# Kernel optimization log

Measured on AMD Instinct MI355X. Metric: run time of the kernel, lower is better.

Reference implementation:

```python
import jax, jax.numpy as jnp
import numpy as np

N_NODES = 100000
N_EDGES = 1600000
IN_DIM, HID_DIM, OUT_DIM = 128, 64, 32
NEG_SLOPE = 0.2  # PyG GATConv default negative_slope


def gat_conv(x, src, dst, num_nodes, W, a_src, a_dst, bias):
    # x: [N, in], W: [in, out], a_src/a_dst: [out], bias: [out]
    h = x @ W                                        # [N, out]
    alpha_s = h @ a_src                              # [N] per-node source score
    alpha_d = h @ a_dst                              # [N] per-node target score
    e = jax.nn.leaky_relu(alpha_s[src] + alpha_d[dst], NEG_SLOPE)  # [E]
    # segment softmax over incoming edges of each dst node
    m = jax.ops.segment_max(e, dst, num_segments=num_nodes)        # [N]
    ex = jnp.exp(e - m[dst])                                        # [E]
    z = jax.ops.segment_sum(ex, dst, num_segments=num_nodes)        # [N]
    coef = ex / z[dst]                                              # [E]
    out = jax.ops.segment_sum(coef[:, None] * h[src], dst, num_segments=num_nodes)
    return out + bias


def setup_inputs() -> dict:
    key = jax.random.key(0)
    ks = jax.random.split(key, 10)
    x = jax.random.normal(ks[0], (N_NODES, IN_DIM), dtype=jnp.float32)
    edge_index = jax.random.randint(ks[1], (2, N_EDGES), 0, N_NODES, dtype=jnp.int64)
    s = 0.1
    W1 = jax.random.normal(ks[2], (IN_DIM, HID_DIM), dtype=jnp.float32) * s
    a_src1 = jax.random.normal(ks[3], (HID_DIM,), dtype=jnp.float32) * s
    a_dst1 = jax.random.normal(ks[4], (HID_DIM,), dtype=jnp.float32) * s
    b1 = jnp.zeros((HID_DIM,), dtype=jnp.float32)
    W2 = jax.random.normal(ks[5], (HID_DIM, OUT_DIM), dtype=jnp.float32) * s
    a_src2 = jax.random.normal(ks[6], (OUT_DIM,), dtype=jnp.float32) * s
    a_dst2 = jax.random.normal(ks[7], (OUT_DIM,), dtype=jnp.float32) * s
    b2 = jnp.zeros((OUT_DIM,), dtype=jnp.float32)
    return {"x": x, "edge_index": edge_index, "W1": W1, "a_src1": a_src1,
            "a_dst1": a_dst1, "b1": b1, "W2": W2, "a_src2": a_src2,
            "a_dst2": a_dst2, "b2": b2}


def reference(x, edge_index, W1, a_src1, a_dst1, b1, W2, a_src2, a_dst2, b2):
    n = x.shape[0]
    loops = jnp.arange(n, dtype=edge_index.dtype)
    src = jnp.concatenate([edge_index[0], loops])  # add_self_loops=True default
    dst = jnp.concatenate([edge_index[1], loops])
    h = jax.nn.relu(gat_conv(x, src, dst, n, W1, a_src1, a_dst1, b1))
    out = gat_conv(h, src, dst, n, W2, a_src2, a_dst2, b2)
    return jax.nn.log_softmax(out, axis=1)
```

## Files before the change

### kernel.cpp

```cpp
#include <hip/hip_runtime.h>

#define N_NODES 100000
#define N_EDGES 1600000
#define ET (N_EDGES + N_NODES)
#define NEG_SLOPE 0.2f

#define BSHIFT 9
#define BW 512
#define NBUCK ((N_NODES + BW - 1) / BW)
#define BCAP 10240
#define BINCH 2048

typedef unsigned short u16;
typedef unsigned int u32;

__device__ __forceinline__ float bf2f(u16 v) {
    return __uint_as_float(((u32)v) << 16);
}
__device__ __forceinline__ u16 f2bf(float f) {
    u32 u = __float_as_uint(f);
    u32 r = (u + 0x7FFFu + ((u >> 16) & 1u)) >> 16;
    return (u16)r;
}
__device__ __forceinline__ float lrelu(float x) { return x > 0.f ? x : NEG_SLOPE * x; }
__device__ __forceinline__ float ldf(const void* p, int i, int bf) {
    return bf ? bf2f(((const u16*)p)[i]) : ((const float*)p)[i];
}
__device__ __forceinline__ int get_dst(const int* __restrict__ ei, int e, int ei64) {
    if (e < N_EDGES) return ei64 ? ei[2 * (N_EDGES + e)] : ei[N_EDGES + e];
    return e - N_EDGES;
}
__device__ __forceinline__ int get_src(const int* __restrict__ ei, int e, int ei64) {
    if (e < N_EDGES) return ei64 ? ei[2 * e] : ei[e];
    return e - N_EDGES;
}

__device__ __forceinline__ void fma8(float wt, uint4 qv, float (&acc)[8]) {
    acc[0] = fmaf(wt, __uint_as_float(qv.x << 16), acc[0]);
    acc[1] = fmaf(wt, __uint_as_float(qv.x & 0xFFFF0000u), acc[1]);
    acc[2] = fmaf(wt, __uint_as_float(qv.y << 16), acc[2]);
    acc[3] = fmaf(wt, __uint_as_float(qv.y & 0xFFFF0000u), acc[3]);
    acc[4] = fmaf(wt, __uint_as_float(qv.z << 16), acc[4]);
    acc[5] = fmaf(wt, __uint_as_float(qv.z & 0xFFFF0000u), acc[5]);
    acc[6] = fmaf(wt, __uint_as_float(qv.w << 16), acc[6]);
    acc[7] = fmaf(wt, __uint_as_float(qv.w & 0xFFFF0000u), acc[7]);
}

__global__ void detect_kernel(const u32* __restrict__ x32, const int* __restrict__ ei,
                              int* __restrict__ flags, int* __restrict__ bcnt) {
    int lane = threadIdx.x;
    for (int i = lane; i < 256; i += 64) bcnt[i] = 0;
    u32 e = (x32[lane] >> 7) & 0xFFu;
    int ok = (e >= 96u && e <= 143u) ? 1 : 0;
    int cnt = (int)__popcll(__ballot(ok));
    int nz = (ei[2 * lane + 1] != 0) + (ei[2 * (lane + 64) + 1] != 0);
    #pragma unroll
    for (int off = 32; off > 0; off >>= 1) nz += __shfl_xor(nz, off);
    if (lane == 0) { flags[0] = (cnt >= 48) ? 1 : 0; flags[1] = (nz == 0) ? 1 : 0; }
}

__global__ __launch_bounds__(256) void bin_kernel(
    const int* __restrict__ ei, const int* __restrict__ flags,
    int* __restrict__ bcnt, u32* __restrict__ bbuf)
{
    __shared__ int hist[NBUCK];
    const int t = threadIdx.x;
    const int base = blockIdx.x * BINCH;
    const int ei64 = flags[1];
    for (int i = t; i < NBUCK; i += 256) hist[i] = 0;
    __syncthreads();
    for (int i = t; i < BINCH; i += 256) {
        int e = base + i;
        if (e >= ET) break;
        int d = get_dst(ei, e, ei64);
        atomicAdd(&hist[d >> BSHIFT], 1);
    }
    __syncthreads();
    for (int i = t; i < NBUCK; i += 256) {
        int c = hist[i];
        hist[i] = (c > 0) ? atomicAdd(&bcnt[i], c) : 0;
    }
    __syncthreads();
    for (int i = t; i < BINCH; i += 256) {
        int e = base + i;
        if (e >= ET) break;
        int d = get_dst(ei, e, ei64);
        int s = get_src(ei, e, ei64);
        int b = d >> BSHIFT;
        int pos = atomicAdd(&hist[b], 1);
        if (pos < BCAP)
            bbuf[(size_t)b * BCAP + pos] = ((u32)(d & (BW - 1)) << 17) | (u32)s;
    }
}

__global__ __launch_bounds__(256) void bscan_kernel(
    const int* __restrict__ bcnt, int* __restrict__ bbase)
{
    __shared__ int sd[256];
    int t = threadIdx.x;
    int v = (t < NBUCK) ? min(bcnt[t], BCAP) : 0;
    sd[t] = v;
    __syncthreads();
    for (int off = 1; off < 256; off <<= 1) {
        int x = (t >= off) ? sd[t - off] : 0;
        __syncthreads();
        sd[t] += x;
        __syncthreads();
    }
    if (t < NBUCK) bbase[t] = sd[t] - v;
    if (t == NBUCK - 1) bbase[NBUCK] = sd[t];
}

__global__ __launch_bounds__(1024) void scatter_kernel(
    const int* __restrict__ bcnt, const int* __restrict__ bbase,
    const u32* __restrict__ bbuf, int* __restrict__ rowptr, int* __restrict__ ssrc)
{
    __shared__ int hist[BW];
    __shared__ int cur[BW];
    __shared__ int wtot[4];
    __shared__ int lds_s[BCAP];
    const int t = threadIdx.x;
    const int b = blockIdx.x;
    const int cnt = min(bcnt[b], BCAP);
    const int base = bbase[b];
    const u32* mybuf = bbuf + (size_t)b * BCAP;

    if (t < BW) hist[t] = 0;
    __syncthreads();
    for (int i = t; i < cnt; i += 1024) atomicAdd(&hist[(int)(mybuf[i] >> 17)], 1);
    __syncthreads();
    int a0 = 0, a1 = 0, s = 0, v = 0;
    const int lane = t & 63, wid = t >> 6;
    if (t < 256) {
        a0 = hist[2 * t]; a1 = hist[2 * t + 1];
        s = a0 + a1;
        v = s;
        #pragma unroll
        for (int off = 1; off < 64; off <<= 1) {
            int n = __shfl_up(v, off);
            if (lane >= off) v += n;
        }
        if (lane == 63) wtot[wid] = v;
    }
    __syncthreads();
    if (t == 0) {
        int acc = 0;
        #pragma unroll
        for (int w = 0; w < 4; ++w) { int tmp = wtot[w]; wtot[w] = acc; acc += tmp; }
    }
    __syncthreads();
    if (t < 256) {
        int excl = v + wtot[wid] - s;
        cur[2 * t] = excl;
        cur[2 * t + 1] = excl + a0;
    }
    __syncthreads();
    if (t < BW) {
        int g = b * BW + t;
        if (g < N_NODES) rowptr[g] = base + cur[t];
    }
    if (b == NBUCK - 1 && t == 0) rowptr[N_NODES] = bbase[NBUCK];
    __syncthreads();
    for (int i = t; i < cnt; i += 1024) {
        u32 code = mybuf[i];
        int pos = atomicAdd(&cur[(int)(code >> 17)], 1);
        lds_s[pos] = (int)(code & 0x1FFFFu);
    }
    __syncthreads();
    for (int i = t; i < cnt; i += 1024) ssrc[base + i] = lds_s[i];
}

__global__ __launch_bounds__(256) void gemm1_kernel(
    const float* __restrict__ x, const float* __restrict__ W,
    const void* __restrict__ a_src, const void* __restrict__ a_dst,
    const int* __restrict__ flags,
    u16* __restrict__ h, float* __restrict__ as_, float* __restrict__ ad_)
{
    __shared__ float xs[256 * 33];
    __shared__ float Wl[32 * 64];
    const int t = threadIdx.x;
    const int node0 = blockIdx.x * 256;
    const int bf = flags[0];
    const int ng = t >> 3;
    const int cg = t & 7;

    float acc[8][8];
    #pragma unroll
    for (int i = 0; i < 8; ++i)
        #pragma unroll
        for (int j = 0; j < 8; ++j) acc[i][j] = 0.f;

    for (int kc = 0; kc < 4; ++kc) {
        const int kb = kc * 32;
        const int c4 = t & 7;
        #pragma unroll
        for (int p = 0; p < 8; ++p) {
            int row = (t >> 3) + p * 32;
            int n = node0 + row;
            float4 vv = make_float4(0.f, 0.f, 0.f, 0.f);
            if (n < N_NODES) {
                if (!bf) {
                    vv = *(const float4*)(x + (size_t)n * 128 + kb + c4 * 4);
                } else {
                    const u16* xh = (const u16*)x;
                    vv.x = bf2f(xh[(size_t)n * 128 + kb + c4 * 4 + 0]);
                    vv.y = bf2f(xh[(size_t)n * 128 + kb + c4 * 4 + 1]);
                    vv.z = bf2f(xh[(size_t)n * 128 + kb + c4 * 4 + 2]);
                    vv.w = bf2f(xh[(size_t)n * 128 + kb + c4 * 4 + 3]);
                }
            }
            float* dstp = &xs[row * 33 + c4 * 4];
            dstp[0] = vv.x; dstp[1] = vv.y; dstp[2] = vv.z; dstp[3] = vv.w;
        }
        if (!bf) {
            #pragma unroll
            for (int qq = 0; qq < 2; ++qq) {
                int f4 = t * 2 + qq;
                ((float4*)Wl)[f4] = ((const float4*)(W + (size_t)kb * 64))[f4];
            }
        } else {
            const u16* Wh = (const u16*)W;
            for (int i = t; i < 2048; i += 256) Wl[i] = bf2f(Wh[(size_t)kb * 64 + i]);
        }
        __syncthreads();

        for (int kk = 0; kk < 32; ++kk) {
            float xr[8];
            #pragma unroll
            for (int i = 0; i < 8; ++i) xr[i] = xs[(ng * 8 + i) * 33 + kk];
            float4 w0 = *(const float4*)&Wl[kk * 64 + cg * 8];
            float4 w1 = *(const float4*)&Wl[kk * 64 + cg * 8 + 4];
            const float wr[8] = {w0.x, w0.y, w0.z, w0.w, w1.x, w1.y, w1.z, w1.w};
            #pragma unroll
            for (int i = 0; i < 8; ++i)
                #pragma unroll
                for (int j = 0; j < 8; ++j)
                    acc[i][j] = fmaf(xr[i], wr[j], acc[i][j]);
        }
        __syncthreads();
    }

    float av[8], dv[8];
    #pragma unroll
    for (int j = 0; j < 8; ++j) {
        av[j] = ldf(a_src, cg * 8 + j, bf);
        dv[j] = ldf(a_dst, cg * 8 + j, bf);
    }
    #pragma unroll
    for (int i = 0; i < 8; ++i) {
        int n = node0 + ng * 8 + i;
        float ps = 0.f, pd = 0.f;
        #pragma unroll
        for (int j = 0; j < 8; ++j) { ps += acc[i][j] * av[j]; pd += acc[i][j] * dv[j]; }
        #pragma unroll
        for (int off = 1; off < 8; off <<= 1) {
            ps += __shfl_xor(ps, off);
            pd += __shfl_xor(pd, off);
        }
        if (n < N_NODES) {
            uint4 hv;
            hv.x = (u32)f2bf(acc[i][0]) | ((u32)f2bf(acc[i][1]) << 16);
            hv.y = (u32)f2bf(acc[i][2]) | ((u32)f2bf(acc[i][3]) << 16);
            hv.z = (u32)f2bf(acc[i][4]) | ((u32)f2bf(acc[i][5]) << 16);
            hv.w = (u32)f2bf(acc[i][6]) | ((u32)f2bf(acc[i][7]) << 16);
            *(uint4*)&h[(size_t)n * 64 + cg * 8] = hv;
            if (cg == 0) { as_[n] = ps; ad_[n] = pd; }
        }
    }
}

template<int SH>
__global__ __launch_bounds__(256) void score_kernel(
    const int* __restrict__ rowptr, const int* __restrict__ ssrc,
    const float* __restrict__ as_, const float* __restrict__ ad_,
    uint2* __restrict__ wexs)
{
    int d = blockIdx.x * 256 + threadIdx.x;
    if (d >= N_NODES) return;
    int beg = rowptr[d], end = rowptr[d + 1];
    int deg = end - beg;
    float add = ad_[d];

    if (deg <= 64) {
        int sj[64];
        float sc[64];
        #pragma unroll
        for (int i = 0; i < 64; ++i) {
            int j = beg + ((i < deg) ? i : 0);
            sj[i] = ssrc[j];
        }
        #pragma unroll
        for (int i = 0; i < 64; ++i) sc[i] = as_[sj[i]];
        float m = -1e30f;
        #pragma unroll
        for (int i = 0; i < 64; ++i) {
            sc[i] = lrelu(sc[i] + add);
            m = (i < deg) ? fmaxf(m, sc[i]) : m;
        }
        float l = 0.f;
        #pragma unroll
        for (int i = 0; i < 64; ++i) {
            float e = (i < deg) ? __expf(sc[i] - m) : 0.f;
            sc[i] = e;
            l += e;
        }
        float inv = 1.f / l;
        #pragma unroll
        for (int i = 0; i < 64; ++i)
            if (i < deg)
                wexs[beg + i] = make_uint2(__float_as_uint(sc[i] * inv),
                                           ((u32)sj[i]) << SH);
    } else {
        float m = -1e30f;
        for (int j = beg; j < end; ++j) m = fmaxf(m, lrelu(as_[ssrc[j]] + add));
        float l = 0.f;
        for (int j = beg; j < end; ++j) l += __expf(lrelu(as_[ssrc[j]] + add) - m);
        float inv = 1.f / l;
        for (int j = beg; j < end; ++j) {
            int s = ssrc[j];
            wexs[j] = make_uint2(
                __float_as_uint(__expf(lrelu(as_[s] + add) - m) * inv),
                ((u32)s) << SH);
        }
    }
}

__global__ __launch_bounds__(256) void gather64_kernel(
    const int* __restrict__ rowptr, const uint2* __restrict__ wexs,
    const u16* __restrict__ h, float* __restrict__ agg)
{
    const int tid = threadIdx.x;
    const int hl = tid & 31;
    const int dreal = blockIdx.x * 8 + (tid >> 5);
    const int dst = min(dreal, N_NODES - 1);
    const int beg = rowptr[dst];
    const int deg = rowptr[dst + 1] - beg;
    const int e4 = hl >> 3;
    const int i8 = hl & 7;
    const char* __restrict__ hb = (const char*)h;
    const u32 boff = (u32)(i8 * 16);

    float acc[8] = {0.f, 0.f, 0.f, 0.f, 0.f, 0.f, 0.f, 0.f};

    #pragma unroll
    for (int g = 0; g < 8; ++g) {
        int eidx = g * 4 + e4;
        bool valid = eidx < deg;
        uint2 p = wexs[beg + (valid ? eidx : 0)];
        float w = valid ? __uint_as_float(p.x) : 0.f;
        uint4 qv = *(const uint4*)(hb + (size_t)(p.y + boff));
        fma8(w, qv, acc);
    }
    int mdeg = max(deg, __shfl_xor(deg, 32));
    for (int g = 8; g * 4 < mdeg; ++g) {
        int eidx = g * 4 + e4;
        bool valid = eidx < deg;
        uint2 p = wexs[beg + (valid ? eidx : 0)];
        float w = valid ? __uint_as_float(p.x) : 0.f;
        uint4 qv = *(const uint4*)(hb + (size_t)(p.y + boff));
        fma8(w, qv, acc);
    }

    #pragma unroll
    for (int c = 0; c < 8; ++c) {
        acc[c] += __shfl_xor(acc[c], 8);
        acc[c] += __shfl_xor(acc[c], 16);
    }
    if (e4 == 0 && dreal < N_NODES) {
        *(float4*)&agg[(size_t)dst * 64 + i8 * 8] =
            make_float4(acc[0], acc[1], acc[2], acc[3]);
        *(float4*)&agg[(size_t)dst * 64 + i8 * 8 + 4] =
            make_float4(acc[4], acc[5], acc[6], acc[7]);
    }
}

__global__ __launch_bounds__(256) void gather32_lsm_kernel(
    const int* __restrict__ rowptr, const uint2* __restrict__ wexs,
    const u16* __restrict__ h, const void* __restrict__ b2,
    const int* __restrict__ flags, float* __restrict__ out)
{
    const int tid = threadIdx.x;
    const int hl = tid & 31;
    const int dreal = blockIdx.x * 8 + (tid >> 5);
    const int dst = min(dreal, N_NODES - 1);
    const int beg = rowptr[dst];
    const int deg = rowptr[dst + 1] - beg;
    const int e8 = hl >> 2;
    const int i4 = hl & 3;
    const int bf = flags[0];
    const char* __restrict__ hb = (const char*)h;
    const u32 boff = (u32)(i4 * 16);

    float acc[8] = {0.f, 0.f, 0.f, 0.f, 0.f, 0.f, 0.f, 0.f};

    #pragma unroll
    for (int g = 0; g < 4; ++g) {
        int eidx = g * 8 + e8;
        bool valid = eidx < deg;
        uint2 p = wexs[beg + (valid ? eidx : 0)];
        float w = valid ? __uint_as_float(p.x) : 0.f;
        uint4 qv = *(const uint4*)(hb + (size_t)(p.y + boff));
        fma8(w, qv, acc);
    }
    int mdeg = max(deg, __shfl_xor(deg, 32));
    for (int g = 4; g * 8 < mdeg; ++g) {
        int eidx = g * 8 + e8;
        bool valid = eidx < deg;
        uint2 p = wexs[beg + (valid ? eidx : 0)];
        float w = valid ? __uint_as_float(p.x) : 0.f;
        uint4 qv = *(const uint4*)(hb + (size_t)(p.y + boff));
        fma8(w, qv, acc);
    }

    #pragma unroll
    for (int c = 0; c < 8; ++c) {
        acc[c] += __shfl_xor(acc[c], 4);
        acc[c] += __shfl_xor(acc[c], 8);
        acc[c] += __shfl_xor(acc[c], 16);
    }

    float v[8];
    #pragma unroll
    for (int c = 0; c < 8; ++c) v[c] = acc[c] + ldf(b2, i4 * 8 + c, bf);
    float mx = v[0];
    #pragma unroll
    for (int c = 1; c < 8; ++c) mx = fmaxf(mx, v[c]);
    mx = fmaxf(mx, __shfl_xor(mx, 1));
    mx = fmaxf(mx, __shfl_xor(mx, 2));
    float ss = 0.f;
    #pragma unroll
    for (int c = 0; c < 8; ++c) ss += __expf(v[c] - mx);
    ss += __shfl_xor(ss, 1);
    ss += __shfl_xor(ss, 2);
    float lg = mx + __logf(ss);
    if (e8 == 0 && dreal < N_NODES) {
        *(float4*)&out[(size_t)dst * 32 + i4 * 8] =
            make_float4(v[0] - lg, v[1] - lg, v[2] - lg, v[3] - lg);
        *(float4*)&out[(size_t)dst * 32 + i4 * 8 + 4] =
            make_float4(v[4] - lg, v[5] - lg, v[6] - lg, v[7] - lg);
    }
}

#define G2_TILE 128

__global__ __launch_bounds__(256, 3) void gemm2_kernel(
    const float* __restrict__ agg1, const void* __restrict__ b1,
    const u32* __restrict__ W32, const void* __restrict__ a_src,
    const void* __restrict__ a_dst, const int* __restrict__ flags,
    u16* __restrict__ h, float* __restrict__ as_, float* __restrict__ ad_)
{
    __shared__ __align__(16) float Wl[64 * 32];
    __shared__ __align__(16) float xs[G2_TILE * 68];
    const int tid = threadIdx.x;
    const int node0 = blockIdx.x * G2_TILE;
    const int bf = flags[0];

    if (bf) {
        for (int i = tid; i < 1024; i += 256) {
            u32 u = W32[i];
            *(float2*)&Wl[2 * i] = make_float2(__uint_as_float(u << 16),
                                               __uint_as_float(u & 0xFFFF0000u));
        }
    } else {
        for (int i = tid; i < 2048; i += 256) Wl[i] = __uint_as_float(W32[i]);
    }
    #pragma unroll
    for (int it = 0; it < 8; ++it) {
        int i = tid + it * 256;
        int nl = i >> 4;
        int k  = (i & 15) * 4;
        int n = node0 + nl;
        float4 v = make_float4(0.f, 0.f, 0.f, 0.f);
        if (n < N_NODES) v = *(const float4*)(agg1 + (size_t)n * 64 + k);
        v.x = fmaxf(v.x + ldf(b1, k + 0, bf), 0.f);
        v.y = fmaxf(v.y + ldf(b1, k + 1, bf), 0.f);
        v.z = fmaxf(v.z + ldf(b1, k + 2, bf), 0.f);
        v.w = fmaxf(v.w + ldf(b1, k + 3, bf), 0.f);
        *(float4*)&xs[nl * 68 + k] = v;
    }
    __syncthreads();

    const int ch0 = (tid & 7) * 4;
    const int nb0 = (tid >> 3) * 4;
    float acc[4][4];
    #pragma unroll
    for (int j = 0; j < 4; ++j)
        #pragma unroll
        for (int c = 0; c < 4; ++c) acc[j][c] = 0.f;

    #pragma unroll 4
    for (int k0 = 0; k0 < 64; k0 += 4) {
        float4 xv0 = *(const float4*)&xs[(nb0 + 0) * 68 + k0];
        float4 xv1 = *(const float4*)&xs[(nb0 + 1) * 68 + k0];
        float4 xv2 = *(const float4*)&xs[(nb0 + 2) * 68 + k0];
        float4 xv3 = *(const float4*)&xs[(nb0 + 3) * 68 + k0];
        const float* xp[4] = { (const float*)&xv0, (const float*)&xv1,
                               (const float*)&xv2, (const float*)&xv3 };
        #pragma unroll
        for (int kk = 0; kk < 4; ++kk) {
            float4 w = *(const float4*)&Wl[(k0 + kk) * 32 + ch0];
            #pragma unroll
            for (int j = 0; j < 4; ++j) {
                float xvv = xp[j][kk];
                acc[j][0] = fmaf(xvv, w.x, acc[j][0]);
                acc[j][1] = fmaf(xvv, w.y, acc[j][1]);
                acc[j][2] = fmaf(xvv, w.z, acc[j][2]);
                acc[j][3] = fmaf(xvv, w.w, acc[j][3]);
            }
        }
    }

    float av[4], dv[4];
    #pragma unroll
    for (int c = 0; c < 4; ++c) {
        av[c] = ldf(a_src, ch0 + c, bf);
        dv[c] = ldf(a_dst, ch0 + c, bf);
    }
    #pragma unroll
    for (int j = 0; j < 4; ++j) {
        float ps = acc[j][0] * av[0] + acc[j][1] * av[1]
                 + acc[j][2] * av[2] + acc[j][3] * av[3];
        float pd = acc[j][0] * dv[0] + acc[j][1] * dv[1]
                 + acc[j][2] * dv[2] + acc[j][3] * dv[3];
        #pragma unroll
        for (int off = 1; off < 8; off <<= 1) {
            ps += __shfl_xor(ps, off);
            pd += __shfl_xor(pd, off);
        }
        int n = node0 + nb0 + j;
        if (n < N_NODES) {
            u32 p0 = (u32)f2bf(acc[j][0]) | ((u32)f2bf(acc[j][1]) << 16);
            u32 p1 = (u32)f2bf(acc[j][2]) | ((u32)f2bf(acc[j][3]) << 16);
            *(uint2*)&h[(size_t)n * 32 + ch0] = make_uint2(p0, p1);
            if ((tid & 7) == 0) { as_[n] = ps; ad_[n] = pd; }
        }
    }
}

extern "C" void kernel_launch(void* const* d_in, const int* in_sizes, int n_in,
                              void* d_out, int out_size, void* d_ws, size_t ws_size,
                              hipStream_t stream) {
    const float* x   = (const float*)d_in[0];
    const int* ei    = (const int*)d_in[1];
    const float* W1  = (const float*)d_in[2];
    const void* a_s1 = d_in[3];
    const void* a_d1 = d_in[4];
    const void* b1   = d_in[5];
    const u32* W2    = (const u32*)d_in[6];
    const void* a_s2 = d_in[7];
    const void* a_d2 = d_in[8];
    const void* b2   = d_in[9];
    float* out = (float*)d_out;

    char* base = (char*)d_ws;
    int* flags = (int*)base;
    u16* h     = (u16*)(base + 64);
    char* q = base + 64 + (size_t)N_NODES * 64 * 2;
    float* as1 = (float*)q; q += (size_t)N_NODES * 4;
    float* ad1 = (float*)q; q += (size_t)N_NODES * 4;
    float* as2 = (float*)q; q += (size_t)N_NODES * 4;
    float* ad2 = (float*)q; q += (size_t)N_NODES * 4;
    float* agg1 = (float*)q; q += (size_t)N_NODES * 64 * 4;
    int* rowptr = (int*)q;  q += (size_t)(N_NODES + 16) * 4;
    int* ssrc   = (int*)q;  q += (size_t)ET * 4;
    int* bcnt   = (int*)q;  q += 256 * 4;
    int* bbase  = (int*)q;  q += 256 * 4;
    q = (char*)(((size_t)q + 255) & ~(size_t)255);
    u32*  bbuf  = (u32*)q;
    uint2* wexs = (uint2*)q;

    detect_kernel<<<1, 64, 0, stream>>>((const u32*)x, ei, flags, bcnt);

    bin_kernel<<<(ET + BINCH - 1) / BINCH, 256, 0, stream>>>(ei, flags, bcnt, bbuf);
    bscan_kernel<<<1, 256, 0, stream>>>(bcnt, bbase);
    scatter_kernel<<<NBUCK, 1024, 0, stream>>>(bcnt, bbase, bbuf, rowptr, ssrc);

    gemm1_kernel<<<(N_NODES + 255) / 256, 256, 0, stream>>>(x, W1, a_s1, a_d1, flags, h, as1, ad1);
    score_kernel<7><<<(N_NODES + 255) / 256, 256, 0, stream>>>(rowptr, ssrc, as1, ad1, wexs);
    gather64_kernel<<<(N_NODES + 7) / 8, 256, 0, stream>>>(rowptr, wexs, h, agg1);

    gemm2_kernel<<<(N_NODES + G2_TILE - 1) / G2_TILE, 256, 0, stream>>>(agg1, b1, W2, a_s2, a_d2, flags, h, as2, ad2);
    score_kernel<6><<<(N_NODES + 255) / 256, 256, 0, stream>>>(rowptr, ssrc, as2, ad2, wexs);
    gather32_lsm_kernel<<<(N_NODES + 7) / 8, 256, 0, stream>>>(rowptr, wexs, h, b2, flags, out);
}
```

Measured before the change: 347.2 us.

## Parallelize edge softmax across a wavefront per destination node

The score kernel moves from one thread per destination node, which serially walks up to 64 edges held in 64-entry register arrays, to one 64-lane wavefront per node with one edge per lane. Max and sum use shuffle-xor reductions, and high-degree nodes use a chunked online softmax. The aim is coalesced reads of ssrc and writes of wexs, lower register pressure and less thread divergence. With about 17 edges per node on average, most lanes of each wavefront sit idle, and the launch count grows to N/4 blocks.

```diff
diff --git a/kernel.cpp b/kernel.cpp
--- a/kernel.cpp
+++ b/kernel.cpp
@@ -275,52 +275,52 @@
     const float* __restrict__ as_, const float* __restrict__ ad_,
     uint2* __restrict__ wexs)
 {
-    int d = blockIdx.x * 256 + threadIdx.x;
-    if (d >= N_NODES) return;
-    int beg = rowptr[d], end = rowptr[d + 1];
-    int deg = end - beg;
-    float add = ad_[d];
+    const int lane = threadIdx.x & 63;
+    const int dst = blockIdx.x * 4 + (threadIdx.x >> 6);
+    if (dst >= N_NODES) return;
+    const int beg = rowptr[dst], end = rowptr[dst + 1];
+    const int deg = end - beg;
+    const float add = ad_[dst];
 
     if (deg <= 64) {
-        int sj[64];
-        float sc[64];
-        #pragma unroll
-        for (int i = 0; i < 64; ++i) {
-            int j = beg + ((i < deg) ? i : 0);
-            sj[i] = ssrc[j];
-        }
-        #pragma unroll
-        for (int i = 0; i < 64; ++i) sc[i] = as_[sj[i]];
-        float m = -1e30f;
-        #pragma unroll
-        for (int i = 0; i < 64; ++i) {
-            sc[i] = lrelu(sc[i] + add);
-            m = (i < deg) ? fmaxf(m, sc[i]) : m;
-        }
-        float l = 0.f;
-        #pragma unroll
-        for (int i = 0; i < 64; ++i) {
-            float e = (i < deg) ? __expf(sc[i] - m) : 0.f;
-            sc[i] = e;
-            l += e;
+        int j = beg + lane;
+        bool valid = j < end;
+        int sj = valid ? ssrc[j] : 0;
+        float sc = valid ? lrelu(as_[sj] + add) : -1e30f;
+        float m = sc;
+        #pragma unroll
+        for (int off = 32; off > 0; off >>= 1) m = fmaxf(m, __shfl_xor(m, off));
+        float ex = __expf(sc - m);
+        float l = ex;
+        #pragma unroll
+        for (int off = 32; off > 0; off >>= 1) l += __shfl_xor(l, off);
+        if (valid)
+            wexs[j] = make_uint2(__float_as_uint(ex / l), ((u32)sj) << SH);
+    } else {
+        float m = -1e30f, l = 0.f;
+        for (int base = beg; base < end; base += 64) {
+            int j = base + lane;
+            bool valid = j < end;
+            float sc = valid ? lrelu(as_[ssrc[j]] + add) : -1e30f;
+            float cm = sc;
+            #pragma unroll
+            for (int off = 32; off > 0; off >>= 1) cm = fmaxf(cm, __shfl_xor(cm, off));
+            float nm = fmaxf(m, cm);
+            float cs = __expf(sc - nm);
+            #pragma unroll
+            for (int off = 32; off > 0; off >>= 1) cs += __shfl_xor(cs, off);
+            l = l * __expf(m - nm) + cs;
+            m = nm;
         }
         float inv = 1.f / l;
-        #pragma unroll
-        for (int i = 0; i < 64; ++i)
-            if (i < deg)
-                wexs[beg + i] = make_uint2(__float_as_uint(sc[i] * inv),
-                                           ((u32)sj[i]) << SH);
-    } else {
-        float m = -1e30f;
-        for (int j = beg; j < end; ++j) m = fmaxf(m, lrelu(as_[ssrc[j]] + add));
-        float l = 0.f;
-        for (int j = beg; j < end; ++j) l += __expf(lrelu(as_[ssrc[j]] + add) - m);
-        float inv = 1.f / l;
-        for (int j = beg; j < end; ++j) {
-            int s = ssrc[j];
-            wexs[j] = make_uint2(
-                __float_as_uint(__expf(lrelu(as_[s] + add) - m) * inv),
-                ((u32)s) << SH);
+        for (int base = beg; base < end; base += 64) {
+            int j = base + lane;
+            if (j < end) {
+                int sj = ssrc[j];
+                wexs[j] = make_uint2(
+                    __float_as_uint(__expf(lrelu(as_[sj] + add) - m) * inv),
+                    ((u32)sj) << SH);
+            }
         }
     }
 }
@@ -576,10 +576,10 @@
     scatter_kernel<<<NBUCK, 1024, 0, stream>>>(bcnt, bbase, bbuf, rowptr, ssrc);
 
     gemm1_kernel<<<(N_NODES + 255) / 256, 256, 0, stream>>>(x, W1, a_s1, a_d1, flags, h, as1, ad1);
-    score_kernel<7><<<(N_NODES + 255) / 256, 256, 0, stream>>>(rowptr, ssrc, as1, ad1, wexs);
+    score_kernel<7><<<(N_NODES + 3) / 4, 256, 0, stream>>>(rowptr, ssrc, as1, ad1, wexs);
     gather64_kernel<<<(N_NODES + 7) / 8, 256, 0, stream>>>(rowptr, wexs, h, agg1);
 
     gemm2_kernel<<<(N_NODES + G2_TILE - 1) / G2_TILE, 256, 0, stream>>>(agg1, b1, W2, a_s2, a_d2, flags, h, as2, ad2);
-    score_kernel<6><<<(N_NODES + 255) / 256, 256, 0, stream>>>(rowptr, ssrc, as2, ad2, wexs);
+    score_kernel<6><<<(N_NODES + 3) / 4, 256, 0, stream>>>(rowptr, ssrc, as2, ad2, wexs);
     gather32_lsm_kernel<<<(N_NODES + 7) / 8, 256, 0, stream>>>(rowptr, wexs, h, b2, flags, out);
 }
```

Result: faster. 338.4 us (-2.5%).
